# Kernel tuning notes

Hardware: AMD Instinct MI355X
Metric: run time of the kernel (lower is better)

Reference implementation:

```python
import jax, jax.numpy as jnp
from jax import lax
import numpy as np

N = 2048          # number of nodes
D = 512           # feature dim
NUM_SUPER = 512   # target number of super-nodes
THRESHOLD = 0.0   # jaccard similarity threshold (0.0 so merging actually runs to completion)
EPS = 1e-10


def _find(parent, i):
    # union-find root lookup (no path compression; equivalence classes are
    # identical to the torch version which only uses path *halving*)
    return lax.while_loop(lambda p: parent[p] != p, lambda p: parent[p], i)


def _build_P(A):
    """Faithful jax version of graph_coarsening_vn's assignment-matrix build.
    Returns P of fixed shape [N, NUM_SUPER] (with threshold=0 the union-find is
    guaranteed to perform exactly N - NUM_SUPER merges, so all NUM_SUPER
    columns are populated and the shape is static)."""
    n = N
    A_bin = (A > 0).astype(jnp.float32)
    deg = A_bin.sum(axis=1)                              # [n]
    inter = A_bin @ A_bin.T                              # [n,n] shared-neighbor counts
    union = deg[:, None] + deg[None, :] - inter
    union = jnp.where(union == 0, EPS, union)
    jac = inter / union                                  # [n,n] jaccard matrix

    iu, ju = jnp.triu_indices(n, k=1)                    # all i<j pairs
    sims = jac[iu, ju]
    valid = sims >= THRESHOLD
    # invalid pairs sort to the end and are gated off (torch drops them entirely)
    keyed = jnp.where(valid, sims, -jnp.inf)
    order = jnp.argsort(-keyed, stable=True)             # descending, stable ties like list.sort
    pi = iu[order].astype(jnp.int32)
    pj = ju[order].astype(jnp.int32)
    ok_arr = valid[order]
    target = jnp.int32(n - NUM_SUPER)

    def step(carry, xs):
        parent, merged = carry
        i, j, ok = xs
        ri = _find(parent, i)
        rj = _find(parent, j)
        do = ok & (ri != rj) & (merged < target)
        parent = jnp.where(do, parent.at[rj].set(ri), parent)
        merged = merged + do.astype(jnp.int32)
        return (parent, merged), None

    init = (jnp.arange(n, dtype=jnp.int32), jnp.int32(0))
    (parent, merged), _ = lax.scan(step, init, (pi, pj, ok_arr))

    idx = jnp.arange(n, dtype=jnp.int32)
    roots = jax.vmap(_find, in_axes=(None, 0))(parent, idx)   # final root per node

    # relabel roots to 0..NUM_SUPER-1 in order of first occurrence (matches
    # the torch `mapping` dict built by scanning i = 0..n-1)
    fo = jax.ops.segment_min(idx, roots, num_segments=n)      # first node index per root
    is_first = (fo[roots] == idx)
    pos_label = jnp.cumsum(is_first.astype(jnp.int32)) - 1
    lab_root = jax.ops.segment_min(pos_label, roots, num_segments=n)
    labels = lab_root[roots]                                  # [n] in [0, NUM_SUPER)

    P_prime = jax.nn.one_hot(labels, NUM_SUPER, dtype=jnp.float32)  # [n, m]
    sizes = P_prime.sum(axis=0)
    P = P_prime / jnp.sqrt(sizes + EPS)[None, :]              # P_prime @ D^{-1/2}
    return P


def setup_inputs() -> dict:
    key = jax.random.key(0)
    kx, ka = jax.random.split(key)
    X = jax.random.normal(kx, (N, D), dtype=jnp.float32)
    U = jax.random.uniform(ka, (N, N), dtype=jnp.float32)
    S = U + U.T                                               # symmetric scores
    A = (S > 1.859).astype(jnp.float32)
    A = A * (1.0 - jnp.eye(N, dtype=jnp.float32))             # zero diagonal
    return {"X": X, "A": A}


def reference(X, A):
    P = _build_P(A)
    X_coarse = P.T @ X          # [NUM_SUPER, D]
    A_coarse = P.T @ A @ P      # [NUM_SUPER, NUM_SUPER]
    return (X_coarse, A_coarse, P)
```

## Files before the change

### kernel.cpp

```cpp
#include <hip/hip_runtime.h>

#define NN 2048
#define WW 32
#define DD 512
#define MS 512
#define TGTM 1536
#define KSH 14
#define KMAX16 16384u
#define CB 128
#define CT 1024
#define ASL 64
#define MSL 128
#define OUTF4 393216

typedef unsigned long long ull;
typedef unsigned short u16;

__device__ __forceinline__ void atomicMin64(ull* p, ull v){
  ull old = *p;
  while (v < old){
    ull assumed = old;
    old = atomicCAS(p, assumed, v);
    if (old == assumed) break;
  }
}
__device__ __forceinline__ unsigned uf_find(unsigned* par, unsigned x){
  while (true){
    unsigned p = par[x];
    if (p == x) return x;
    unsigned g = par[p];
    if (g == p) return p;
    par[x] = g;
    x = g;
  }
}
__device__ __forceinline__ void uf_union(unsigned* par, unsigned x, unsigned y){
  while (true){
    unsigned rx = uf_find(par, x), ry = uf_find(par, y);
    if (rx == ry) return;
    if (rx > ry){ unsigned tm = rx; rx = ry; ry = tm; }
    if (atomicCAS(&par[ry], ry, rx) == ry) return;
    x = rx; y = ry;
  }
}
__device__ __forceinline__ unsigned block_scan_incl(unsigned v, unsigned* partials, int t){
  int lane = t & 63, wv = t >> 6;
  unsigned x = v;
  #pragma unroll
  for (int off = 1; off < 64; off <<= 1){
    unsigned n = __shfl_up(x, off, 64);
    if (lane >= off) x += n;
  }
  __syncthreads();
  if (lane == 63) partials[wv] = x;
  __syncthreads();
  if (wv == 0){
    unsigned p = (lane < 16) ? partials[lane] : 0u;
    #pragma unroll
    for (int off = 1; off < 16; off <<= 1){
      unsigned n = __shfl_up(p, off, 64);
      if (lane >= off) p += n;
    }
    if (lane < 16) partials[lane] = p;
  }
  __syncthreads();
  if (wv > 0) x += partials[wv-1];
  return x;
}
__device__ __forceinline__ void gbar(unsigned* cnt, unsigned target, int t){
  __syncthreads();
  if (t == 0){
    __threadfence();
    __hip_atomic_fetch_add(cnt, 1u, __ATOMIC_RELEASE, __HIP_MEMORY_SCOPE_AGENT);
    while (__hip_atomic_load(cnt, __ATOMIC_RELAXED, __HIP_MEMORY_SCOPE_AGENT) < target)
      __builtin_amdgcn_s_sleep(1);
    __threadfence();
  }
  __syncthreads();
}

__global__ void k_build(const float* __restrict__ A, ull* __restrict__ bits,
                        unsigned* __restrict__ deg, unsigned* __restrict__ bar,
                        float* __restrict__ out){
  int gid = blockIdx.x*blockDim.x + threadIdx.x;
  float4 z4 = make_float4(0.f,0.f,0.f,0.f);
  float4* o4 = (float4*)out;
  for (unsigned idx = (unsigned)gid; idx < OUTF4; idx += 65536u) o4[idx] = z4;
  if (threadIdx.x == 0) atomicCAS(bar, 0xAAAAAAAAu, 0u);
  int i = gid >> 5, w = gid & 31;
  const float4* row = (const float4*)(A + ((size_t)i << 11) + (w << 6));
  ull m = 0ull;
  #pragma unroll
  for (int k = 0; k < 16; ++k){
    float4 v = row[k];
    if (v.x > 0.0f) m |= (1ull << (4*k+0));
    if (v.y > 0.0f) m |= (1ull << (4*k+1));
    if (v.z > 0.0f) m |= (1ull << (4*k+2));
    if (v.w > 0.0f) m |= (1ull << (4*k+3));
  }
  bits[((size_t)i << 5) + w] = m;
  unsigned p = (unsigned)__popcll(m);
  #pragma unroll
  for (int off = 16; off; off >>= 1) p += __shfl_xor(p, off, 32);
  if (w == 0) deg[i] = p;
}

__global__ void k_keymat(const ull* __restrict__ bits,
                         const unsigned* __restrict__ deg, u16* __restrict__ keyM){
  __shared__ ull bi[64][33];
  __shared__ ull bj[64][33];
  __shared__ unsigned degi[64], degj[64];
  int ib = blockIdx.x, jb = blockIdx.y;
  int t = threadIdx.x;
  for (int idx = t; idx < 64*32; idx += 256){
    int r = idx >> 5, w = idx & 31;
    bi[r][w] = bits[(((size_t)(ib*64 + r)) << 5) + w];
    bj[r][w] = bits[(((size_t)(jb*64 + r)) << 5) + w];
  }
  if (t < 64){ degi[t] = deg[ib*64 + t]; degj[t] = deg[jb*64 + t]; }
  __syncthreads();
  int tr = (t >> 4) << 2;
  int tc = (t & 15) << 2;
  unsigned inter[4][4];
  #pragma unroll
  for (int r = 0; r < 4; ++r)
    #pragma unroll
    for (int c = 0; c < 4; ++c) inter[r][c] = 0u;
  #pragma unroll 8
  for (int w = 0; w < 32; ++w){
    ull a0 = bi[tr+0][w], a1 = bi[tr+1][w], a2 = bi[tr+2][w], a3 = bi[tr+3][w];
    ull b0 = bj[tc+0][w], b1 = bj[tc+1][w], b2 = bj[tc+2][w], b3 = bj[tc+3][w];
    inter[0][0] += (unsigned)__popcll(a0 & b0);
    inter[0][1] += (unsigned)__popcll(a0 & b1);
    inter[0][2] += (unsigned)__popcll(a0 & b2);
    inter[0][3] += (unsigned)__popcll(a0 & b3);
    inter[1][0] += (unsigned)__popcll(a1 & b0);
    inter[1][1] += (unsigned)__popcll(a1 & b1);
    inter[1][2] += (unsigned)__popcll(a1 & b2);
    inter[1][3] += (unsigned)__popcll(a1 & b3);
    inter[2][0] += (unsigned)__popcll(a2 & b0);
    inter[2][1] += (unsigned)__popcll(a2 & b1);
    inter[2][2] += (unsigned)__popcll(a2 & b2);
    inter[2][3] += (unsigned)__popcll(a2 & b3);
    inter[3][0] += (unsigned)__popcll(a3 & b0);
    inter[3][1] += (unsigned)__popcll(a3 & b1);
    inter[3][2] += (unsigned)__popcll(a3 & b2);
    inter[3][3] += (unsigned)__popcll(a3 & b3);
  }
  #pragma unroll
  for (int r = 0; r < 4; ++r){
    int i = ib*64 + tr + r;
    u16 kv[4];
    #pragma unroll
    for (int c = 0; c < 4; ++c){
      int j = jb*64 + tc + c;
      unsigned key = 0u;
      if (i != j){
        unsigned iv = inter[r][c];
        unsigned b = degi[tr+r] + degj[tc+c] - iv;
        if (b != 0u){
          unsigned num = (iv << KSH) + (b >> 1);
          key = num / b;
        }
      }
      kv[c] = (u16)key;
    }
    *(ushort4*)(keyM + (((size_t)i) << 11) + (jb*64 + tc)) =
        make_ushort4(kv[0], kv[1], kv[2], kv[3]);
  }
}

__global__ void __launch_bounds__(CT)
k_boruvka(const u16* __restrict__ keyM, ull* __restrict__ node_best ,
          unsigned* __restrict__ bar,
          unsigned* __restrict__ labels_g, float* __restrict__ scale_g,
          unsigned* __restrict__ offs_g, unsigned* __restrict__ memb_g,
          float* __restrict__ P){
  __shared__ ull ed[NN];
  __shared__ ull cbest[NN];
  __shared__ alignas(16) unsigned lab[NN];
  __shared__ unsigned nxtA[NN];
  __shared__ unsigned partials[16];
  __shared__ unsigned selS[4];
  __shared__ unsigned gcntS;
  __shared__ unsigned cntS;
  int t = threadIdx.x;
  int b = blockIdx.x;
  if (t == 0) cntS = 0;
  for (int i = t; i < NN; i += CT) lab[i] = (unsigned)i;
  __syncthreads();

  for (int round = 0; round < 11; ++round){
    ull* nb = node_best + ((round & 1) ? NN : 0);
    for (int c = t; c < NN; c += CT){ cbest[c] = ~0ull; nxtA[c] = (unsigned)c; }
    {
      int i = b*(CT/64) + (t >> 6);
      int lane = t & 63;
      unsigned ci = lab[i];
      const u16* row = keyM + ((size_t)i << 11);
      ull best = ~0ull;
      #pragma unroll
      for (int it = 0; it < 8; ++it){
        int j0 = it*256 + lane*4;
        ushort4 k4 = *(const ushort4*)(row + j0);
        uint4   c4 = *(const uint4*)(lab + j0);
        #pragma unroll
        for (int q = 0; q < 4; ++q){
          int j = j0 + q;
          unsigned key = (q==0)?k4.x:(q==1)?k4.y:(q==2)?k4.z:k4.w;
          unsigned cj  = (q==0)?c4.x:(q==1)?c4.y:(q==2)?c4.z:c4.w;
          if (j == i || cj == ci) continue;
          unsigned kp = KMAX16 - key;
          unsigned a  = (i < j) ? (unsigned)i : (unsigned)j;
          unsigned b2 = (i < j) ? (unsigned)j : (unsigned)i;
          ull v = (((ull)kp) << 22) | (((ull)a) << 11) | b2;
          if (v < best) best = v;
        }
      }
      for (int off = 32; off; off >>= 1){
        ull o = __shfl_xor(best, off);
        if (o < best) best = o;
      }
      if (lane == 0) nb[i] = best;
    }
    gbar(bar, (unsigned)(round + 1) * (unsigned)CB, t);
    for (int i = t; i < NN; i += CT) atomicMin64(&cbest[lab[i]], nb[i]);
    __syncthreads();
    for (int c = t; c < NN; c += CT){
      ull v = cbest[c];
      if (v == ~0ull) continue;
      unsigned a = (unsigned)((v >> 11) & 2047u), b2 = (unsigned)(v & 2047u);
      unsigned la = lab[a], lb = lab[b2];
      if (la == lb) continue;
      unsigned other = (la == (unsigned)c) ? lb : la;
      if (!(cbest[other] == v && other < (unsigned)c)){
        unsigned idx = atomicAdd(&cntS, 1u);
        if (idx < (unsigned)NN) ed[idx] = v;
      }
      uf_union(nxtA, la, lb);
    }
    __syncthreads();
    for (int i = t; i < NN; i += CT) lab[i] = uf_find(nxtA, lab[i]);
    __syncthreads();
    if (cntS >= (unsigned)(NN-1)) break;
  }
  if (b != 0) return;

  unsigned cnt = cntS; if (cnt > (unsigned)NN) cnt = NN;
  unsigned* h1 = lab;
  unsigned* h2 = lab + 256;
  for (int k = t; k < 129+256; k += CT) if (k < 129 || k >= 256) lab[k] = 0u;
  if (t < 128) h2[t] = 0u;
  if (t == 0){ selS[0] = 128u; selS[1] = 1u; selS[2] = 127u; selS[3] = 1u; gcntS = 0u; }
  __syncthreads();
  for (int e = t; e < (int)cnt; e += CT) atomicAdd(&h1[(unsigned)(ed[e] >> 29)], 1u);
  __syncthreads();
  if (t == 0){
    unsigned c = 0;
    for (unsigned bk = 0; bk <= 128; ++bk){
      if (c + h1[bk] >= (unsigned)TGTM){ selS[0] = bk; selS[1] = (unsigned)TGTM - c; break; }
      c += h1[bk];
    }
  }
  __syncthreads();
  unsigned B1 = selS[0], r1 = selS[1];
  for (int e = t; e < (int)cnt; e += CT){
    ull v = ed[e];
    if ((unsigned)(v >> 29) == B1) atomicAdd(&h2[(unsigned)((v >> 22) & 127u)], 1u);
  }
  __syncthreads();
  if (t == 0){
    unsigned c = 0;
    for (unsigned bk = 0; bk < 128; ++bk){
      if (c + h2[bk] >= r1){ selS[2] = bk; selS[3] = r1 - c; break; }
      c += h2[bk];
    }
  }
  __syncthreads();
  unsigned B2 = selS[2], r2 = selS[3];
  unsigned kpSel = (B1 << 7) | B2;
  ull* glist = cbest;
  for (int e = t; e < (int)cnt; e += CT){
    ull v = ed[e];
    if ((unsigned)(v >> 22) == kpSel){
      unsigned idx = atomicAdd(&gcntS, 1u);
      glist[idx] = v;
    }
  }
  for (int c = t; c < NN; c += CT) nxtA[c] = (unsigned)c;
  __syncthreads();
  unsigned gc = gcntS;
  for (int e = t; e < (int)cnt; e += CT){
    ull v = ed[e];
    unsigned kp = (unsigned)(v >> 22);
    bool sel;
    if (kp < kpSel) sel = true;
    else if (kp > kpSel) sel = false;
    else {
      unsigned r = 0;
      for (unsigned j = 0; j < gc; ++j) r += (glist[j] < v) ? 1u : 0u;
      sel = (r < r2);
    }
    if (sel){
      unsigned a = (unsigned)((v >> 11) & 2047u), b2 = (unsigned)(v & 2047u);
      uf_union(nxtA, a, b2);
    }
  }
  __syncthreads();
  for (int i = t; i < NN; i += CT) lab[i] = uf_find(nxtA, (unsigned)i);
  __syncthreads();
  unsigned* plab  = (unsigned*)ed;
  unsigned* sizes = (unsigned*)cbest;
  int i0 = 2*t, i1 = 2*t + 1;
  unsigned f0 = (lab[i0] == (unsigned)i0) ? 1u : 0u;
  unsigned f1 = (lab[i1] == (unsigned)i1) ? 1u : 0u;
  unsigned s = f0 + f1;
  unsigned incl = block_scan_incl(s, partials, t);
  plab[i0] = incl - s; plab[i1] = incl - s + f0;
  for (int c = t; c < MS; c += CT) sizes[c] = 0u;
  __syncthreads();
  for (int i = t; i < NN; i += CT){
    unsigned L = plab[lab[i]];
    labels_g[i] = L;
    if (L < (unsigned)MS) atomicAdd(&sizes[L], 1u);
  }
  __syncthreads();
  for (int c = t; c < MS; c += CT) scale_g[c] = 1.0f / sqrtf((float)sizes[c] + 1e-10f);
  unsigned* off_l  = nxtA;
  unsigned* cursor = nxtA + 1024;
  unsigned my = (t < MS) ? sizes[t] : 0u;
  unsigned incl2 = block_scan_incl(my, partials, t);
  if (t < MS){
    unsigned ex = incl2 - my;
    off_l[t] = ex; offs_g[t] = ex;
  }
  if (t == 0) offs_g[MS] = (unsigned)NN;
  __syncthreads();
  for (int c = t; c < MS; c += CT) cursor[c] = off_l[c];
  __syncthreads();
  for (int i = t; i < NN; i += CT){
    unsigned L = plab[lab[i]];
    unsigned pos = atomicAdd(&cursor[L], 1u);
    memb_g[pos] = (unsigned)i;
  }
  for (int i = t; i < NN; i += CT){
    unsigned L = plab[lab[i]];
    P[((size_t)i << 9) + L] = 1.0f / sqrtf((float)sizes[L] + 1e-10f);
  }
}

__global__ void k_coarse(const float* __restrict__ X, const ull* __restrict__ bits,
                         const unsigned* __restrict__ labels,
                         const unsigned* __restrict__ offs, const unsigned* __restrict__ memb,
                         const float* __restrict__ scale,
                         float* __restrict__ Xc, float* __restrict__ Ac){
  int c = blockIdx.x, y = blockIdx.y, t = threadIdx.x;
  unsigned o0 = offs[c], e = offs[c+1];
  if (y < 32){
    __shared__ unsigned mlist[MSL];
    int dtile = y >> 4, sl = y & 15;
    unsigned o = o0 + (unsigned)sl*(unsigned)MSL;
    if (o >= e) return;
    int nm = (int)min((unsigned)MSL, e - o);
    if (t < nm) mlist[t] = memb[o + t];
    __syncthreads();
    int d = dtile*256 + t;
    float a0=0.f,a1=0.f,a2=0.f,a3=0.f,a4=0.f,a5=0.f,a6=0.f,a7=0.f;
    int k = 0;
    for (; k + 8 <= nm; k += 8){
      a0 += X[((size_t)mlist[k+0] << 9) + d];
      a1 += X[((size_t)mlist[k+1] << 9) + d];
      a2 += X[((size_t)mlist[k+2] << 9) + d];
      a3 += X[((size_t)mlist[k+3] << 9) + d];
      a4 += X[((size_t)mlist[k+4] << 9) + d];
      a5 += X[((size_t)mlist[k+5] << 9) + d];
      a6 += X[((size_t)mlist[k+6] << 9) + d];
      a7 += X[((size_t)mlist[k+7] << 9) + d];
    }
    for (; k < nm; ++k) a0 += X[((size_t)mlist[k] << 9) + d];
    float acc = (((a0+a1)+(a2+a3)) + ((a4+a5)+(a6+a7))) * scale[c];
    if (e - o0 <= (unsigned)MSL) Xc[((size_t)c << 9) + d] = acc;
    else atomicAdd(&Xc[((size_t)c << 9) + d], acc);
  } else {
    __shared__ float row[MS];
    __shared__ unsigned labS[NN];
    __shared__ unsigned mlistA[ASL];
    int sl = y - 32;
    unsigned o = o0 + (unsigned)sl*(unsigned)ASL;
    if (o >= e) return;
    int nm = (int)min((unsigned)ASL, e - o);
    for (int j = t; j < MS; j += 256) row[j] = 0.0f;
    for (int i = t; i < NN; i += 256) labS[i] = labels[i];
    if (t < nm) mlistA[t] = memb[o + t];
    __syncthreads();
    for (int idx = t; idx < nm*WW; idx += 256){
      unsigned m = mlistA[idx >> 5];
      int w = idx & 31;
      ull word = bits[((size_t)m << 5) + w];
      while (word){
        int bb = __ffsll((long long)word) - 1;
        unsigned j = (unsigned)(w*64 + bb);
        atomicAdd(&row[labS[j]], 1.0f);
        word &= word - 1ull;
      }
    }
    __syncthreads();
    float sc = scale[c];
    bool single = (e - o0) <= (unsigned)ASL;
    if (single){
      for (int j = t; j < MS; j += 256)
        Ac[((size_t)c << 9) + j] = row[j] * sc * scale[j];
    } else {
      for (int j = t; j < MS; j += 256){
        float v = row[j];
        if (v != 0.0f) atomicAdd(&Ac[((size_t)c << 9) + j], v * sc * scale[j]);
      }
    }
  }
}

extern "C" void kernel_launch(void* const* d_in, const int* in_sizes, int n_in,
                              void* d_out, int out_size, void* d_ws, size_t ws_size,
                              hipStream_t stream) {
  const float* X = (const float*)d_in[0];
  const float* A = (const float*)d_in[1];
  float* out = (float*)d_out;
  char* ws = (char*)d_ws;
  ull*      bits     = (ull*)     (ws + 0x000000);
  unsigned* deg      = (unsigned*)(ws + 0x080000);
  ull*      nodebest = (ull*)     (ws + 0x084000);
  unsigned* labels   = (unsigned*)(ws + 0x08D000);
  float*    scale    = (float*)   (ws + 0x08F000);
  unsigned* bar      = (unsigned*)(ws + 0x08F800);
  unsigned* memb     = (unsigned*)(ws + 0x084000);
  unsigned* offs     = (unsigned*)(ws + 0x080000);
  u16*      keyM     = (u16*)     (ws + 0x090000);

  float* Xc = out;
  float* Ac = out + MS*MS;
  float* P  = out + 2*MS*MS;

  k_build<<<(NN*WW)/256, 256, 0, stream>>>(A, bits, deg, bar, out);
  k_keymat<<<dim3(NN/64, NN/64), 256, 0, stream>>>(bits, deg, keyM);

  void* args[] = { (void*)&keyM, (void*)&nodebest, (void*)&bar,
                   (void*)&labels, (void*)&scale, (void*)&offs, (void*)&memb, (void*)&P };
  hipLaunchCooperativeKernel((void*)k_boruvka, dim3(CB), dim3(CT), args, 0, stream);

  k_coarse<<<dim3(MS, 57), 256, 0, stream>>>(X, bits, labels, offs, memb, scale, Xc, Ac);
}
```

Baseline: 250.0 us.

## Fuse coarsening pass into cooperative Boruvka kernel and use native 64-bit atomicMin

Removes the separate k_coarse launch and performs the X and A coarsening inside the cooperative Boruvka kernel after an extra grid barrier, with 128 blocks looping over the work items. The CAS-loop atomicMin64 is replaced by the native 64-bit atomicMin on shared memory. Workspace offsets move so memb and offs no longer alias node_best and deg. The aim is to save one launch and its gap. The cost is that the coarsening now runs on only 128 blocks instead of 512x57, with per-item __syncthreads.

```diff
diff --git a/kernel.cpp b/kernel.cpp
--- a/kernel.cpp
+++ b/kernel.cpp
@@ -16,14 +16,6 @@
 typedef unsigned long long ull;
 typedef unsigned short u16;
 
-__device__ __forceinline__ void atomicMin64(ull* p, ull v){
-  ull old = *p;
-  while (v < old){
-    ull assumed = old;
-    old = atomicCAS(p, assumed, v);
-    if (old == assumed) break;
-  }
-}
 __device__ __forceinline__ unsigned uf_find(unsigned* par, unsigned x){
   while (true){
     unsigned p = par[x];
@@ -171,11 +163,12 @@
 }
 
 __global__ void __launch_bounds__(CT)
-k_boruvka(const u16* __restrict__ keyM, ull* __restrict__ node_best ,
+k_boruvka(const u16* __restrict__ keyM, const float* __restrict__ X,
+          const ull* __restrict__ bits, ull* __restrict__ node_best ,
           unsigned* __restrict__ bar,
           unsigned* __restrict__ labels_g, float* __restrict__ scale_g,
           unsigned* __restrict__ offs_g, unsigned* __restrict__ memb_g,
-          float* __restrict__ P){
+          float* __restrict__ out){
   __shared__ ull ed[NN];
   __shared__ ull cbest[NN];
   __shared__ alignas(16) unsigned lab[NN];
@@ -186,6 +179,10 @@
   __shared__ unsigned cntS;
   int t = threadIdx.x;
   int b = blockIdx.x;
+  unsigned ep = 0;
+  float* Xc = out;
+  float* Ac = out + MS*MS;
+  float* P  = out + 2*MS*MS;
   if (t == 0) cntS = 0;
   for (int i = t; i < NN; i += CT) lab[i] = (unsigned)i;
   __syncthreads();
@@ -223,8 +220,8 @@
       }
       if (lane == 0) nb[i] = best;
     }
-    gbar(bar, (unsigned)(round + 1) * (unsigned)CB, t);
-    for (int i = t; i < NN; i += CT) atomicMin64(&cbest[lab[i]], nb[i]);
+    gbar(bar, (++ep)*(unsigned)CB, t);
+    for (int i = t; i < NN; i += CT) atomicMin(&cbest[lab[i]], nb[i]);
     __syncthreads();
     for (int c = t; c < NN; c += CT){
       ull v = cbest[c];
@@ -244,177 +241,186 @@
     __syncthreads();
     if (cntS >= (unsigned)(NN-1)) break;
   }
-  if (b != 0) return;
-
-  unsigned cnt = cntS; if (cnt > (unsigned)NN) cnt = NN;
-  unsigned* h1 = lab;
-  unsigned* h2 = lab + 256;
-  for (int k = t; k < 129+256; k += CT) if (k < 129 || k >= 256) lab[k] = 0u;
-  if (t < 128) h2[t] = 0u;
-  if (t == 0){ selS[0] = 128u; selS[1] = 1u; selS[2] = 127u; selS[3] = 1u; gcntS = 0u; }
-  __syncthreads();
-  for (int e = t; e < (int)cnt; e += CT) atomicAdd(&h1[(unsigned)(ed[e] >> 29)], 1u);
-  __syncthreads();
-  if (t == 0){
-    unsigned c = 0;
-    for (unsigned bk = 0; bk <= 128; ++bk){
-      if (c + h1[bk] >= (unsigned)TGTM){ selS[0] = bk; selS[1] = (unsigned)TGTM - c; break; }
-      c += h1[bk];
-    }
-  }
-  __syncthreads();
-  unsigned B1 = selS[0], r1 = selS[1];
-  for (int e = t; e < (int)cnt; e += CT){
-    ull v = ed[e];
-    if ((unsigned)(v >> 29) == B1) atomicAdd(&h2[(unsigned)((v >> 22) & 127u)], 1u);
-  }
-  __syncthreads();
-  if (t == 0){
-    unsigned c = 0;
-    for (unsigned bk = 0; bk < 128; ++bk){
-      if (c + h2[bk] >= r1){ selS[2] = bk; selS[3] = r1 - c; break; }
-      c += h2[bk];
-    }
-  }
-  __syncthreads();
-  unsigned B2 = selS[2], r2 = selS[3];
-  unsigned kpSel = (B1 << 7) | B2;
-  ull* glist = cbest;
-  for (int e = t; e < (int)cnt; e += CT){
-    ull v = ed[e];
-    if ((unsigned)(v >> 22) == kpSel){
-      unsigned idx = atomicAdd(&gcntS, 1u);
-      glist[idx] = v;
-    }
-  }
-  for (int c = t; c < NN; c += CT) nxtA[c] = (unsigned)c;
-  __syncthreads();
-  unsigned gc = gcntS;
-  for (int e = t; e < (int)cnt; e += CT){
-    ull v = ed[e];
-    unsigned kp = (unsigned)(v >> 22);
-    bool sel;
-    if (kp < kpSel) sel = true;
-    else if (kp > kpSel) sel = false;
-    else {
-      unsigned r = 0;
-      for (unsigned j = 0; j < gc; ++j) r += (glist[j] < v) ? 1u : 0u;
-      sel = (r < r2);
-    }
-    if (sel){
-      unsigned a = (unsigned)((v >> 11) & 2047u), b2 = (unsigned)(v & 2047u);
-      uf_union(nxtA, a, b2);
-    }
-  }
-  __syncthreads();
-  for (int i = t; i < NN; i += CT) lab[i] = uf_find(nxtA, (unsigned)i);
-  __syncthreads();
-  unsigned* plab  = (unsigned*)ed;
-  unsigned* sizes = (unsigned*)cbest;
-  int i0 = 2*t, i1 = 2*t + 1;
-  unsigned f0 = (lab[i0] == (unsigned)i0) ? 1u : 0u;
-  unsigned f1 = (lab[i1] == (unsigned)i1) ? 1u : 0u;
-  unsigned s = f0 + f1;
-  unsigned incl = block_scan_incl(s, partials, t);
-  plab[i0] = incl - s; plab[i1] = incl - s + f0;
-  for (int c = t; c < MS; c += CT) sizes[c] = 0u;
-  __syncthreads();
-  for (int i = t; i < NN; i += CT){
-    unsigned L = plab[lab[i]];
-    labels_g[i] = L;
-    if (L < (unsigned)MS) atomicAdd(&sizes[L], 1u);
-  }
-  __syncthreads();
-  for (int c = t; c < MS; c += CT) scale_g[c] = 1.0f / sqrtf((float)sizes[c] + 1e-10f);
-  unsigned* off_l  = nxtA;
-  unsigned* cursor = nxtA + 1024;
-  unsigned my = (t < MS) ? sizes[t] : 0u;
-  unsigned incl2 = block_scan_incl(my, partials, t);
-  if (t < MS){
-    unsigned ex = incl2 - my;
-    off_l[t] = ex; offs_g[t] = ex;
-  }
-  if (t == 0) offs_g[MS] = (unsigned)NN;
-  __syncthreads();
-  for (int c = t; c < MS; c += CT) cursor[c] = off_l[c];
-  __syncthreads();
-  for (int i = t; i < NN; i += CT){
-    unsigned L = plab[lab[i]];
-    unsigned pos = atomicAdd(&cursor[L], 1u);
-    memb_g[pos] = (unsigned)i;
-  }
-  for (int i = t; i < NN; i += CT){
-    unsigned L = plab[lab[i]];
-    P[((size_t)i << 9) + L] = 1.0f / sqrtf((float)sizes[L] + 1e-10f);
-  }
-}
-
-__global__ void k_coarse(const float* __restrict__ X, const ull* __restrict__ bits,
-                         const unsigned* __restrict__ labels,
-                         const unsigned* __restrict__ offs, const unsigned* __restrict__ memb,
-                         const float* __restrict__ scale,
-                         float* __restrict__ Xc, float* __restrict__ Ac){
-  int c = blockIdx.x, y = blockIdx.y, t = threadIdx.x;
-  unsigned o0 = offs[c], e = offs[c+1];
-  if (y < 32){
-    __shared__ unsigned mlist[MSL];
-    int dtile = y >> 4, sl = y & 15;
-    unsigned o = o0 + (unsigned)sl*(unsigned)MSL;
-    if (o >= e) return;
-    int nm = (int)min((unsigned)MSL, e - o);
-    if (t < nm) mlist[t] = memb[o + t];
-    __syncthreads();
-    int d = dtile*256 + t;
-    float a0=0.f,a1=0.f,a2=0.f,a3=0.f,a4=0.f,a5=0.f,a6=0.f,a7=0.f;
-    int k = 0;
-    for (; k + 8 <= nm; k += 8){
-      a0 += X[((size_t)mlist[k+0] << 9) + d];
-      a1 += X[((size_t)mlist[k+1] << 9) + d];
-      a2 += X[((size_t)mlist[k+2] << 9) + d];
-      a3 += X[((size_t)mlist[k+3] << 9) + d];
-      a4 += X[((size_t)mlist[k+4] << 9) + d];
-      a5 += X[((size_t)mlist[k+5] << 9) + d];
-      a6 += X[((size_t)mlist[k+6] << 9) + d];
-      a7 += X[((size_t)mlist[k+7] << 9) + d];
-    }
-    for (; k < nm; ++k) a0 += X[((size_t)mlist[k] << 9) + d];
-    float acc = (((a0+a1)+(a2+a3)) + ((a4+a5)+(a6+a7))) * scale[c];
-    if (e - o0 <= (unsigned)MSL) Xc[((size_t)c << 9) + d] = acc;
-    else atomicAdd(&Xc[((size_t)c << 9) + d], acc);
-  } else {
-    __shared__ float row[MS];
-    __shared__ unsigned labS[NN];
-    __shared__ unsigned mlistA[ASL];
-    int sl = y - 32;
-    unsigned o = o0 + (unsigned)sl*(unsigned)ASL;
-    if (o >= e) return;
-    int nm = (int)min((unsigned)ASL, e - o);
-    for (int j = t; j < MS; j += 256) row[j] = 0.0f;
-    for (int i = t; i < NN; i += 256) labS[i] = labels[i];
-    if (t < nm) mlistA[t] = memb[o + t];
-    __syncthreads();
-    for (int idx = t; idx < nm*WW; idx += 256){
-      unsigned m = mlistA[idx >> 5];
-      int w = idx & 31;
-      ull word = bits[((size_t)m << 5) + w];
-      while (word){
-        int bb = __ffsll((long long)word) - 1;
-        unsigned j = (unsigned)(w*64 + bb);
-        atomicAdd(&row[labS[j]], 1.0f);
-        word &= word - 1ull;
-      }
-    }
-    __syncthreads();
-    float sc = scale[c];
-    bool single = (e - o0) <= (unsigned)ASL;
-    if (single){
-      for (int j = t; j < MS; j += 256)
-        Ac[((size_t)c << 9) + j] = row[j] * sc * scale[j];
-    } else {
-      for (int j = t; j < MS; j += 256){
-        float v = row[j];
-        if (v != 0.0f) atomicAdd(&Ac[((size_t)c << 9) + j], v * sc * scale[j]);
-      }
+
+  if (b == 0){
+    unsigned cnt = cntS; if (cnt > (unsigned)NN) cnt = NN;
+    unsigned* h1 = lab;
+    unsigned* h2 = lab + 256;
+    for (int k = t; k < 129+256; k += CT) if (k < 129 || k >= 256) lab[k] = 0u;
+    if (t < 128) h2[t] = 0u;
+    if (t == 0){ selS[0] = 128u; selS[1] = 1u; selS[2] = 127u; selS[3] = 1u; gcntS = 0u; }
+    __syncthreads();
+    for (int e = t; e < (int)cnt; e += CT) atomicAdd(&h1[(unsigned)(ed[e] >> 29)], 1u);
+    __syncthreads();
+    if (t == 0){
+      unsigned c = 0;
+      for (unsigned bk = 0; bk <= 128; ++bk){
+        if (c + h1[bk] >= (unsigned)TGTM){ selS[0] = bk; selS[1] = (unsigned)TGTM - c; break; }
+        c += h1[bk];
+      }
+    }
+    __syncthreads();
+    unsigned B1 = selS[0], r1 = selS[1];
+    for (int e = t; e < (int)cnt; e += CT){
+      ull v = ed[e];
+      if ((unsigned)(v >> 29) == B1) atomicAdd(&h2[(unsigned)((v >> 22) & 127u)], 1u);
+    }
+    __syncthreads();
+    if (t == 0){
+      unsigned c = 0;
+      for (unsigned bk = 0; bk < 128; ++bk){
+        if (c + h2[bk] >= r1){ selS[2] = bk; selS[3] = r1 - c; break; }
+        c += h2[bk];
+      }
+    }
+    __syncthreads();
+    unsigned B2 = selS[2], r2 = selS[3];
+    unsigned kpSel = (B1 << 7) | B2;
+    ull* glist = cbest;
+    for (int e = t; e < (int)cnt; e += CT){
+      ull v = ed[e];
+      if ((unsigned)(v >> 22) == kpSel){
+        unsigned idx = atomicAdd(&gcntS, 1u);
+        glist[idx] = v;
+      }
+    }
+    for (int c = t; c < NN; c += CT) nxtA[c] = (unsigned)c;
+    __syncthreads();
+    unsigned gc = gcntS;
+    for (int e = t; e < (int)cnt; e += CT){
+      ull v = ed[e];
+      unsigned kp = (unsigned)(v >> 22);
+      bool sel;
+      if (kp < kpSel) sel = true;
+      else if (kp > kpSel) sel = false;
+      else {
+        unsigned r = 0;
+        for (unsigned j = 0; j < gc; ++j) r += (glist[j] < v) ? 1u : 0u;
+        sel = (r < r2);
+      }
+      if (sel){
+        unsigned a = (unsigned)((v >> 11) & 2047u), b2 = (unsigned)(v & 2047u);
+        uf_union(nxtA, a, b2);
+      }
+    }
+    __syncthreads();
+    for (int i = t; i < NN; i += CT) lab[i] = uf_find(nxtA, (unsigned)i);
+    __syncthreads();
+    unsigned* plab  = (unsigned*)ed;
+    unsigned* sizes = (unsigned*)cbest;
+    int i0 = 2*t, i1 = 2*t + 1;
+    unsigned f0 = (lab[i0] == (unsigned)i0) ? 1u : 0u;
+    unsigned f1 = (lab[i1] == (unsigned)i1) ? 1u : 0u;
+    unsigned s = f0 + f1;
+    unsigned incl = block_scan_incl(s, partials, t);
+    plab[i0] = incl - s; plab[i1] = incl - s + f0;
+    for (int c = t; c < MS; c += CT) sizes[c] = 0u;
+    __syncthreads();
+    for (int i = t; i < NN; i += CT){
+      unsigned L = plab[lab[i]];
+      labels_g[i] = L;
+      if (L < (unsigned)MS) atomicAdd(&sizes[L], 1u);
+    }
+    __syncthreads();
+    for (int c = t; c < MS; c += CT) scale_g[c] = 1.0f / sqrtf((float)sizes[c] + 1e-10f);
+    unsigned* off_l  = nxtA;
+    unsigned* cursor = nxtA + 1024;
+    unsigned my = (t < MS) ? sizes[t] : 0u;
+    unsigned incl2 = block_scan_incl(my, partials, t);
+    if (t < MS){
+      unsigned ex = incl2 - my;
+      off_l[t] = ex; offs_g[t] = ex;
+    }
+    if (t == 0) offs_g[MS] = (unsigned)NN;
+    __syncthreads();
+    for (int c = t; c < MS; c += CT) cursor[c] = off_l[c];
+    __syncthreads();
+    for (int i = t; i < NN; i += CT){
+      unsigned L = plab[lab[i]];
+      unsigned pos = atomicAdd(&cursor[L], 1u);
+      memb_g[pos] = (unsigned)i;
+    }
+    for (int i = t; i < NN; i += CT){
+      unsigned L = plab[lab[i]];
+      P[((size_t)i << 9) + L] = 1.0f / sqrtf((float)sizes[L] + 1e-10f);
+    }
+  }
+  gbar(bar, (++ep)*(unsigned)CB, t);
+
+  {
+    unsigned* labS   = lab;
+    float*    scaleS = (float*)nxtA;
+    unsigned* offsS  = nxtA + 512;
+    unsigned* mlist  = nxtA + 1032;
+    float*    spadX  = (float*)cbest;
+    float*    rowA   = ((float*)cbest) + 512;
+    for (int i = t; i < NN; i += CT) labS[i] = labels_g[i];
+    for (int c = t; c < MS; c += CT) scaleS[c] = scale_g[c];
+    for (int c = t; c <= MS; c += CT) offsS[c] = offs_g[c];
+    __syncthreads();
+    for (int item = b; item < MS*16; item += CB){
+      int c = item >> 4, sl = item & 15;
+      unsigned o0 = offsS[c], e = offsS[c+1];
+      unsigned o = o0 + (unsigned)sl*(unsigned)MSL;
+      if (o >= e) continue;
+      int nm = (int)min((unsigned)MSL, e - o);
+      if (t < nm) mlist[t] = memb_g[o + t];
+      __syncthreads();
+      int d = t & 511, h = t >> 9;
+      int nm2 = nm >> 1;
+      int lo = h ? nm2 : 0, hi = h ? nm : nm2;
+      float a0=0.f,a1=0.f,a2=0.f,a3=0.f,a4=0.f,a5=0.f,a6=0.f,a7=0.f;
+      int k = lo;
+      for (; k + 8 <= hi; k += 8){
+        a0 += X[((size_t)mlist[k+0] << 9) + d];
+        a1 += X[((size_t)mlist[k+1] << 9) + d];
+        a2 += X[((size_t)mlist[k+2] << 9) + d];
+        a3 += X[((size_t)mlist[k+3] << 9) + d];
+        a4 += X[((size_t)mlist[k+4] << 9) + d];
+        a5 += X[((size_t)mlist[k+5] << 9) + d];
+        a6 += X[((size_t)mlist[k+6] << 9) + d];
+        a7 += X[((size_t)mlist[k+7] << 9) + d];
+      }
+      for (; k < hi; ++k) a0 += X[((size_t)mlist[k] << 9) + d];
+      float acc = ((a0+a1)+(a2+a3)) + ((a4+a5)+(a6+a7));
+      if (h == 1) spadX[d] = acc;
+      __syncthreads();
+      if (h == 0){
+        float tot = (acc + spadX[d]) * scaleS[c];
+        if (e - o0 <= (unsigned)MSL) Xc[((size_t)c << 9) + d] = tot;
+        else atomicAdd(&Xc[((size_t)c << 9) + d], tot);
+      }
+      __syncthreads();
+    }
+    for (int item = b; item < MS*32; item += CB){
+      int c = item >> 5, sl = item & 31;
+      unsigned o0 = offsS[c], e = offsS[c+1];
+      unsigned o = o0 + (unsigned)sl*(unsigned)ASL;
+      if (o >= e) continue;
+      int nm = (int)min((unsigned)ASL, e - o);
+      if (t < MS) rowA[t] = 0.0f;
+      if (t < nm) mlist[t] = memb_g[o + t];
+      __syncthreads();
+      for (int idx = t; idx < nm*WW; idx += CT){
+        unsigned m = mlist[idx >> 5];
+        int w = idx & 31;
+        ull word = bits[((size_t)m << 5) + w];
+        while (word){
+          int bb = __ffsll((long long)word) - 1;
+          unsigned j = (unsigned)(w*64 + bb);
+          atomicAdd(&rowA[labS[j]], 1.0f);
+          word &= word - 1ull;
+        }
+      }
+      __syncthreads();
+      if (t < MS){
+        float v = rowA[t];
+        float sc = scaleS[c];
+        bool single = (e - o0) <= (unsigned)ASL;
+        if (single) Ac[((size_t)c << 9) + t] = v * sc * scaleS[t];
+        else if (v != 0.0f) atomicAdd(&Ac[((size_t)c << 9) + t], v * sc * scaleS[t]);
+      }
+      __syncthreads();
     }
   }
 }
@@ -432,20 +438,15 @@
   unsigned* labels   = (unsigned*)(ws + 0x08D000);
   float*    scale    = (float*)   (ws + 0x08F000);
   unsigned* bar      = (unsigned*)(ws + 0x08F800);
-  unsigned* memb     = (unsigned*)(ws + 0x084000);
-  unsigned* offs     = (unsigned*)(ws + 0x080000);
-  u16*      keyM     = (u16*)     (ws + 0x090000);
-
-  float* Xc = out;
-  float* Ac = out + MS*MS;
-  float* P  = out + 2*MS*MS;
+  unsigned* memb     = (unsigned*)(ws + 0x090000);
+  unsigned* offs     = (unsigned*)(ws + 0x092000);
+  u16*      keyM     = (u16*)     (ws + 0x0A0000);
 
   k_build<<<(NN*WW)/256, 256, 0, stream>>>(A, bits, deg, bar, out);
   k_keymat<<<dim3(NN/64, NN/64), 256, 0, stream>>>(bits, deg, keyM);
 
-  void* args[] = { (void*)&keyM, (void*)&nodebest, (void*)&bar,
-                   (void*)&labels, (void*)&scale, (void*)&offs, (void*)&memb, (void*)&P };
+  void* args[] = { (void*)&keyM, (void*)&X, (void*)&bits, (void*)&nodebest, (void*)&bar,
+                   (void*)&labels, (void*)&scale, (void*)&offs, (void*)&memb,
+                   (void*)&out };
   hipLaunchCooperativeKernel((void*)k_boruvka, dim3(CB), dim3(CT), args, 0, stream);
-
-  k_coarse<<<dim3(MS, 57), 256, 0, stream>>>(X, bits, labels, offs, memb, scale, Xc, Ac);
-}
+}
```

Measured after the change: 375.5 us. +50.2%, slower.
